# Performance work log

Hardware: AMD Instinct MI355X
Metric: run time of the kernel (lower is better)

Reference implementation:

```python
import jax, jax.numpy as jnp
import numpy as np

H_DIM = 128
C_DIM = 128


def _linear_params(key, in_dim, out_dim):
    kw, kb = jax.random.split(key)
    bound = 1.0 / np.sqrt(in_dim)
    W = jax.random.uniform(kw, (in_dim, out_dim), minval=-bound, maxval=bound, dtype=jnp.float32)
    b = jax.random.uniform(kb, (out_dim,), minval=-bound, maxval=bound, dtype=jnp.float32)
    return W, b


def setup_inputs() -> dict:
    key = jax.random.key(0)
    kx, kh, kc, k1, k2, k3, k4, k5 = jax.random.split(key, 8)
    B = 262144
    x = jax.random.normal(kx, (B, H_DIM), dtype=jnp.float32)
    h = jax.random.normal(kh, (B, H_DIM), dtype=jnp.float32)
    c = jax.random.normal(kc, (B, C_DIM), dtype=jnp.float32)
    Wf, bf = _linear_params(k1, 2 * H_DIM, H_DIM)
    Wi, bi = _linear_params(k2, 2 * H_DIM, H_DIM)
    Wc, bc = _linear_params(k3, 2 * H_DIM, C_DIM)
    Wo, bo = _linear_params(k4, 2 * H_DIM, H_DIM)
    Wch, bch = _linear_params(k5, C_DIM, H_DIM)
    return {"x": x, "h": h, "c": c,
            "Wf": Wf, "bf": bf, "Wi": Wi, "bi": bi,
            "Wc": Wc, "bc": bc, "Wo": Wo, "bo": bo,
            "Wch": Wch, "bch": bch}


def reference(x, h, c, Wf, bf, Wi, bi, Wc, bc, Wo, bo, Wch, bch):
    concat = jnp.concatenate([x, h], axis=-1)  # [B, 2H]
    # Fuse the four gate projections into one GEMM, then split.
    W_gates = jnp.concatenate([Wf, Wi, Wc, Wo], axis=1)  # [2H, 3H+C]
    b_gates = jnp.concatenate([bf, bi, bc, bo], axis=0)
    gates = concat @ W_gates + b_gates
    f_pre, i_pre, ct_pre, o_pre = jnp.split(
        gates, [H_DIM, 2 * H_DIM, 2 * H_DIM + C_DIM], axis=-1)
    f = jax.nn.sigmoid(f_pre)
    i = jax.nn.sigmoid(i_pre)
    c_tilde = jnp.tanh(ct_pre)
    c_new = f * c + i * c_tilde
    o = jax.nn.sigmoid(o_pre)
    h_new = o * jnp.tanh(c_new @ Wch + bch)
    return (h_new, c_new)
```

## Files before the change

### kernel.cpp

```cpp
#include <hip/hip_runtime.h>
#include <hip/hip_bf16.h>


typedef __attribute__((ext_vector_type(8))) short bf16x8;
typedef __attribute__((ext_vector_type(4))) float f32x4;

#define AB0   0
#define AB1   16384
#define LAND0 32768
#define LAND1 65536
#define CEX0  98304
#define CEX1  106496

static __device__ __forceinline__ unsigned short f2bf(float f) {
    unsigned int u = __builtin_bit_cast(unsigned int, f);
    u += 0x7FFFu + ((u >> 16) & 1u);
    return (unsigned short)(u >> 16);
}

static __device__ __forceinline__ unsigned int cvtpk(float lo, float hi) {
    unsigned int r;
    asm("v_cvt_pk_bf16_f32 %0, %1, %2" : "=v"(r) : "v"(lo), "v"(hi));
    return r;
}

static __device__ __forceinline__ bf16x8 cvt8(f32x4 a, f32x4 b) {
    union { bf16x8 v; unsigned int w[4]; } r;
    r.w[0] = cvtpk(a[0], a[1]);
    r.w[1] = cvtpk(a[2], a[3]);
    r.w[2] = cvtpk(b[0], b[1]);
    r.w[3] = cvtpk(b[2], b[3]);
    return r.v;
}

static __device__ __forceinline__ float fsig(float x) {
    float e = __builtin_amdgcn_exp2f(-1.44269504f * x);
    return __builtin_amdgcn_rcpf(1.0f + e);
}
static __device__ __forceinline__ float ftanh(float x) {
    float e = __builtin_amdgcn_exp2f(2.8853900818f * x);
    return 1.0f - 2.0f * __builtin_amdgcn_rcpf(e + 1.0f);
}

static __device__ __forceinline__ void gload16(const void* gsrc, void* ldst) {
    __builtin_amdgcn_global_load_lds(
        (const __attribute__((address_space(1))) unsigned int*)gsrc,
        (__attribute__((address_space(3))) unsigned int*)ldst,
        16, 0, 0);
}

#define MEMFENCE asm volatile("" ::: "memory")

__global__ void prep_weights(const float* __restrict__ Wf, const float* __restrict__ Wi,
                             const float* __restrict__ Wc, const float* __restrict__ Wo,
                             const float* __restrict__ Wch,
                             unsigned short* __restrict__ WgF,
                             unsigned short* __restrict__ WchF)
{
    int u = blockIdx.x * 256 + threadIdx.x;
    if (u < 16384) {
        int lane = u & 63, g = (u >> 6) & 3, wn = (u >> 8) & 7, ks = u >> 11;
        int l15 = lane & 15, lg = lane >> 4;
        int cg = wn * 16 + l15;
        int k0 = ks * 32 + lg * 8;
        const float* W = (g == 0) ? Wf : (g == 1) ? Wi : (g == 2) ? Wc : Wo;
        union { bf16x8 v; unsigned short s[8]; } r;
#pragma unroll
        for (int i = 0; i < 8; ++i) r.s[i] = f2bf(W[(size_t)(k0 + i) * 128 + cg]);
        *(bf16x8*)(WgF + (size_t)u * 8) = r.v;
    } else if (u < 16384 + 2048) {
        int u2 = u - 16384;
        int lane = u2 & 63, wn = (u2 >> 6) & 7, kt = u2 >> 9;
        int l15 = lane & 15, lg = lane >> 4;
        int col = wn * 16 + l15, k0 = kt * 32 + lg * 8;
        union { bf16x8 v; unsigned short s[8]; } r;
#pragma unroll
        for (int i = 0; i < 8; ++i) r.s[i] = f2bf(Wch[(size_t)(k0 + i) * 128 + col]);
        *(bf16x8*)(WchF + (size_t)u2 * 8) = r.v;
    }
}

#define TILE_BODY(T, CUR, CIN, COUT)                                            \
  do {                                                                          \
    const long m0 = base + (long)(T) * 32;                                      \
                                             \
    if ((T) < 31) {                                                             \
      const char* ln = lds + ((CUR) ? LAND0 : LAND1) + rowA * 1024;             \
      f32x4 q0 = *(const f32x4*)(ln + (((kgA * 4 + 0) ^ swzA) << 4));           \
      f32x4 q1 = *(const f32x4*)(ln + (((kgA * 4 + 1) ^ swzA) << 4));           \
      f32x4 q2 = *(const f32x4*)(ln + (((kgA * 4 + 2) ^ swzA) << 4));           \
      f32x4 q3 = *(const f32x4*)(ln + (((kgA * 4 + 3) ^ swzA) << 4));           \
      char* fb = lds + ((CUR) ? AB0 : AB1);                                     \
      *(bf16x8*)(fb + aoff0) = cvt8(q0, q1);                                    \
      *(bf16x8*)(fb + aoff1) = cvt8(q2, q3);                                    \
    }                                                                           \
    MEMFENCE;                                                                   \
                                \
    if ((T) < 31) {                                                             \
      _Pragma("unroll")                                                         \
      for (int am = 0; am < 2; ++am)                                            \
        _Pragma("unroll")                                                       \
        for (int r = 0; r < 4; ++r)                                             \
          COUT[am * 4 + r] = cg[(m0 + 32 + am * 16 + lg * 4 + r) * 128 + colc]; \
    }                                                                           \
    MEMFENCE;                                                                   \
                                          \
    if ((T) < 30) {                                                             \
      char* ad = lds + ((CUR) ? LAND1 : LAND0) + wn * 1024 + lane * 16;         \
      _Pragma("unroll")                                                         \
      for (int j = 0; j < 4; ++j)                                               \
        gload16(dmaA + (m0 + 64 + wn + j * 8) * 128, ad + j * 8192);            \
    }                                                                           \
    MEMFENCE;                                                                   \
                        \
    {                                                                           \
      const char* ab = lds + ((CUR) ? AB1 : AB0);                               \
      _Pragma("unroll")                                                         \
      for (int ks = 0; ks < 8; ++ks) {                                          \
        bf16x8 af0 = *(const bf16x8*)(ab + ks * 1024 + ((lane * 16) ^ (ks << 4)));       \
        bf16x8 af1 = *(const bf16x8*)(ab + (8 + ks) * 1024 + ((lane * 16) ^ (ks << 4))); \
        _Pragma("unroll")                                                       \
        for (int g_ = 0; g_ < 4; ++g_) {                                        \
          acc[0][g_] = __builtin_amdgcn_mfma_f32_16x16x32_bf16(af0, Breg[ks][g_], acc[0][g_], 0, 0, 0); \
          acc[1][g_] = __builtin_amdgcn_mfma_f32_16x16x32_bf16(af1, Breg[ks][g_], acc[1][g_], 0, 0, 0); \
        }                                                                       \
      }                                                                         \
    }                                                                           \
              \
    {                                                                           \
      char* cexb = lds + ((CUR) ? CEX1 : CEX0);                                 \
      _Pragma("unroll")                                                         \
      for (int am = 0; am < 2; ++am)                                            \
        _Pragma("unroll")                                                       \
        for (int r = 0; r < 4; ++r) {                                           \
          float f_  = fsig(acc[am][0][r] + bfb);                                \
          float i_  = fsig(acc[am][1][r] + bib);                                \
          float ct_ = ftanh(acc[am][2][r] + bcb);                               \
          float cv_ = f_ * CIN[am * 4 + r] + i_ * ct_;                          \
          coutp[(m0 + am * 16 + lg * 4 + r) * 128 + colc] = cv_;                \
          *(unsigned short*)(cexb + (am * 4 + (wn >> 1)) * 1024                 \
               + (cslotbase + lg * 4 + r) * 16 + (l15 & 7) * 2) = f2bf(cv_);    \
        }                                                                       \
    }                                                                           \
       \
    asm volatile("s_waitcnt lgkmcnt(0) vmcnt(8)" ::: "memory");                 \
    __builtin_amdgcn_sched_barrier(0);                                          \
    __builtin_amdgcn_s_barrier();                                               \
    __builtin_amdgcn_sched_barrier(0);                                          \
                                  \
    {                                                                           \
      const char* cexr = lds + ((CUR) ? CEX1 : CEX0);                           \
      f32x4 acc2_0 = {0.f,0.f,0.f,0.f}, acc2_1 = {0.f,0.f,0.f,0.f};             \
      _Pragma("unroll")                                                         \
      for (int kt = 0; kt < 4; ++kt) {                                          \
        bf16x8 p0 = *(const bf16x8*)(cexr + kt * 1024 + lane * 16);             \
        bf16x8 p1 = *(const bf16x8*)(cexr + (4 + kt) * 1024 + lane * 16);       \
        acc2_0 = __builtin_amdgcn_mfma_f32_16x16x32_bf16(p0, Wreg[kt], acc2_0, 0, 0, 0); \
        acc2_1 = __builtin_amdgcn_mfma_f32_16x16x32_bf16(p1, Wreg[kt], acc2_1, 0, 0, 0); \
      }                                                                         \
      _Pragma("unroll")                                                         \
      for (int r = 0; r < 4; ++r) {                                             \
        float o0 = fsig(acc[0][3][r] + bob);                                    \
        houtp[(m0 +      lg * 4 + r) * 128 + colc] = o0 * ftanh(acc2_0[r] + bchb); \
        float o1 = fsig(acc[1][3][r] + bob);                                    \
        houtp[(m0 + 16 + lg * 4 + r) * 128 + colc] = o1 * ftanh(acc2_1[r] + bchb); \
      }                                                                         \
    }                                                                           \
    _Pragma("unroll")                                                           \
    for (int am = 0; am < 2; ++am)                                              \
      _Pragma("unroll")                                                         \
      for (int g_ = 0; g_ < 4; ++g_) acc[am][g_] = (f32x4){0.f,0.f,0.f,0.f};    \
  } while (0)

__global__ __launch_bounds__(512, 2) void lstm_fused(
    const float* __restrict__ xg, const float* __restrict__ hg, const float* __restrict__ cg,
    const float* __restrict__ bfv, const float* __restrict__ biv,
    const float* __restrict__ bcv, const float* __restrict__ bov,
    const float* __restrict__ bchv,
    const unsigned short* __restrict__ WgF, const unsigned short* __restrict__ WchF,
    float* __restrict__ out, int nrows)
{
    __shared__ uint4 lds4[7168];
    char* lds = (char*)lds4;

    const int tid  = threadIdx.x;
    const int lane = tid & 63;
    const int wn   = tid >> 6;
    const int l15  = lane & 15;
    const int lg   = lane >> 4;
    const long base = (long)blockIdx.x << 10;

    float* houtp = out;
    float* coutp = out + (size_t)nrows * 128;

    const int colc = wn * 16 + l15;
    const float bfb = bfv[colc], bib = biv[colc], bcb = bcv[colc],
                bob = bov[colc], bchb = bchv[colc];
    const int cslotbase = ((wn & 1) * 2 + (l15 >> 3)) * 16;

    bf16x8 Breg[8][4];
#pragma unroll
    for (int ks = 0; ks < 8; ++ks)
#pragma unroll
        for (int g = 0; g < 4; ++g)
            Breg[ks][g] = *(const bf16x8*)(WgF + (size_t)((ks * 32 + wn * 4 + g) * 512 + lane * 8));
    bf16x8 Wreg[4];
#pragma unroll
    for (int kt = 0; kt < 4; ++kt)
        Wreg[kt] = *(const bf16x8*)(WchF + (size_t)((kt * 8 + wn) * 512 + lane * 8));

    const int gu = lane ^ wn;
    const float* dmaA = ((gu < 32) ? (xg + gu * 4) : (hg + (gu - 32) * 4));

    const int rowA = tid >> 4;
    const int kgA  = tid & 15;
    const int swzA = rowA & 7;
    const int ksA  = kgA >> 1;
    const int lgA  = (kgA & 1) * 2;
    const int amA  = rowA >> 4;
    const int l15A = rowA & 15;
    const int aoff0 = (amA * 8 + ksA) * 1024 + ((((lgA    ) * 16 + l15A) * 16) ^ (ksA << 4));
    const int aoff1 = (amA * 8 + ksA) * 1024 + ((((lgA + 1) * 16 + l15A) * 16) ^ (ksA << 4));
    const float* asrc = (kgA < 8) ? (xg + kgA * 16) : (hg + (kgA - 8) * 16);

    float c0[8], c1[8];
#pragma unroll
    for (int am = 0; am < 2; ++am)
#pragma unroll
        for (int r = 0; r < 4; ++r)
            c0[am * 4 + r] = cg[(base + am * 16 + lg * 4 + r) * 128 + colc];
    MEMFENCE;
    {
        char* ad = lds + LAND1 + wn * 1024 + lane * 16;
#pragma unroll
        for (int j = 0; j < 4; ++j)
            gload16(dmaA + (base + 32 + wn + j * 8) * 128, ad + j * 8192);
    }
    MEMFENCE;
    {
        const float* s = asrc + (base + rowA) * 128;
        f32x4 v0 = ((const f32x4*)s)[0], v1 = ((const f32x4*)s)[1],
              v2 = ((const f32x4*)s)[2], v3 = ((const f32x4*)s)[3];
        *(bf16x8*)(lds + AB0 + aoff0) = cvt8(v0, v1);
        *(bf16x8*)(lds + AB0 + aoff1) = cvt8(v2, v3);
    }
    asm volatile("s_waitcnt lgkmcnt(0) vmcnt(0)" ::: "memory");
    __builtin_amdgcn_sched_barrier(0);
    __builtin_amdgcn_s_barrier();
    __builtin_amdgcn_sched_barrier(0);

    f32x4 acc[2][4];
#pragma unroll
    for (int am = 0; am < 2; ++am)
#pragma unroll
        for (int g = 0; g < 4; ++g) acc[am][g] = {0.f, 0.f, 0.f, 0.f};

#pragma unroll 1
    for (int t = 0; t < 32; t += 2) {
        TILE_BODY(t,     0, c0, c1);
        TILE_BODY(t + 1, 1, c1, c0);
    }
}

extern "C" void kernel_launch(void* const* d_in, const int* in_sizes, int n_in,
                              void* d_out, int out_size, void* d_ws, size_t ws_size,
                              hipStream_t stream)
{
    const float* x   = (const float*)d_in[0];
    const float* h   = (const float*)d_in[1];
    const float* c   = (const float*)d_in[2];
    const float* Wf  = (const float*)d_in[3];
    const float* bf_ = (const float*)d_in[4];
    const float* Wi  = (const float*)d_in[5];
    const float* bi_ = (const float*)d_in[6];
    const float* Wc  = (const float*)d_in[7];
    const float* bc_ = (const float*)d_in[8];
    const float* Wo  = (const float*)d_in[9];
    const float* bo_ = (const float*)d_in[10];
    const float* Wch = (const float*)d_in[11];
    const float* bch = (const float*)d_in[12];

    unsigned short* WgF  = (unsigned short*)d_ws;
    unsigned short* WchF = WgF + 512 * 256;
    float* out = (float*)d_out;

    int nrows = in_sizes[0] / 128;

    prep_weights<<<dim3(72), dim3(256), 0, stream>>>(Wf, Wi, Wc, Wo, Wch, WgF, WchF);
    lstm_fused<<<dim3(nrows / 1024), dim3(512), 0, stream>>>(
        x, h, c, bf_, bi_, bc_, bo_, bch, WgF, WchF, out, nrows);
}
```

Baseline: 143.4 us.

## Split gate GEMM across 16 waves and exchange activated gates through LDS

Doubles the block to 1024 threads (16 waves). Each wave now computes two 16-column slices of a single gate for 32 rows, where before each wave held all four gates for one column slice. Activated gates are written to LDS as bf16 and regathered per column, so the cell update and output GEMM are split over row halves. The aim is to cut per-wave register pressure, since the weight fragments held per wave drop by half and the Wch weights are now loaded from global inside the loop, and to raise latency hiding. The cost is an extra LDS exchange and barrier per tile, and gate values are rounded to bf16 before the cell update.

```diff
diff --git a/kernel.cpp b/kernel.cpp
--- a/kernel.cpp
+++ b/kernel.cpp
@@ -9,8 +9,8 @@
 #define AB1   16384
 #define LAND0 32768
 #define LAND1 65536
-#define CEX0  98304
-#define CEX1  106496
+#define GEX   98304
+#define CEX   131072
 
 static __device__ __forceinline__ unsigned short f2bf(float f) {
     unsigned int u = __builtin_bit_cast(unsigned int, f);
@@ -33,6 +33,13 @@
     return r.v;
 }
 
+static __device__ __forceinline__ float bf2f_lo(unsigned int u) {
+    return __builtin_bit_cast(float, u << 16);
+}
+static __device__ __forceinline__ float bf2f_hi(unsigned int u) {
+    return __builtin_bit_cast(float, u & 0xFFFF0000u);
+}
+
 static __device__ __forceinline__ float fsig(float x) {
     float e = __builtin_amdgcn_exp2f(-1.44269504f * x);
     return __builtin_amdgcn_rcpf(1.0f + e);
@@ -54,25 +61,27 @@
 __global__ void prep_weights(const float* __restrict__ Wf, const float* __restrict__ Wi,
                              const float* __restrict__ Wc, const float* __restrict__ Wo,
                              const float* __restrict__ Wch,
-                             unsigned short* __restrict__ WgF,
+                             unsigned short* __restrict__ WgF2,
                              unsigned short* __restrict__ WchF)
 {
     int u = blockIdx.x * 256 + threadIdx.x;
     if (u < 16384) {
-        int lane = u & 63, g = (u >> 6) & 3, wn = (u >> 8) & 7, ks = u >> 11;
+        int lane = u & 63, rest = u >> 6;
+        int ks = rest & 7, cf = (rest >> 3) & 1, wvp = rest >> 4;
+        int g1 = wvp & 3, cg = wvp >> 2;
         int l15 = lane & 15, lg = lane >> 4;
-        int cg = wn * 16 + l15;
+        int colg = cg * 32 + cf * 16 + l15;
         int k0 = ks * 32 + lg * 8;
-        const float* W = (g == 0) ? Wf : (g == 1) ? Wi : (g == 2) ? Wc : Wo;
+        const float* W = (g1 == 0) ? Wf : (g1 == 1) ? Wi : (g1 == 2) ? Wc : Wo;
         union { bf16x8 v; unsigned short s[8]; } r;
 #pragma unroll
-        for (int i = 0; i < 8; ++i) r.s[i] = f2bf(W[(size_t)(k0 + i) * 128 + cg]);
-        *(bf16x8*)(WgF + (size_t)u * 8) = r.v;
+        for (int i = 0; i < 8; ++i) r.s[i] = f2bf(W[(size_t)(k0 + i) * 128 + colg]);
+        *(bf16x8*)(WgF2 + (size_t)u * 8) = r.v;
     } else if (u < 16384 + 2048) {
         int u2 = u - 16384;
-        int lane = u2 & 63, wn = (u2 >> 6) & 7, kt = u2 >> 9;
+        int lane = u2 & 63, c8 = (u2 >> 6) & 7, kt = u2 >> 9;
         int l15 = lane & 15, lg = lane >> 4;
-        int col = wn * 16 + l15, k0 = kt * 32 + lg * 8;
+        int col = c8 * 16 + l15, k0 = kt * 32 + lg * 8;
         union { bf16x8 v; unsigned short s[8]; } r;
 #pragma unroll
         for (int i = 0; i < 8; ++i) r.s[i] = f2bf(Wch[(size_t)(k0 + i) * 128 + col]);
@@ -80,180 +89,182 @@
     }
 }
 
-#define TILE_BODY(T, CUR, CIN, COUT)                                            \
+#define TILE_BODY(T, P, CIN, COUT)                                              \
   do {                                                                          \
     const long m0 = base + (long)(T) * 32;                                      \
-                                             \
+         \
     if ((T) < 31) {                                                             \
-      const char* ln = lds + ((CUR) ? LAND0 : LAND1) + rowA * 1024;             \
-      f32x4 q0 = *(const f32x4*)(ln + (((kgA * 4 + 0) ^ swzA) << 4));           \
-      f32x4 q1 = *(const f32x4*)(ln + (((kgA * 4 + 1) ^ swzA) << 4));           \
-      f32x4 q2 = *(const f32x4*)(ln + (((kgA * 4 + 2) ^ swzA) << 4));           \
-      f32x4 q3 = *(const f32x4*)(ln + (((kgA * 4 + 3) ^ swzA) << 4));           \
-      char* fb = lds + ((CUR) ? AB0 : AB1);                                     \
-      *(bf16x8*)(fb + aoff0) = cvt8(q0, q1);                                    \
-      *(bf16x8*)(fb + aoff1) = cvt8(q2, q3);                                    \
+      const char* lnb = lds + ((P) ? LAND0 : LAND1) + rowC * 1024;              \
+      f32x4 q0 = *(const f32x4*)(lnb + (((u0C    ) ^ swzC) << 4));              \
+      f32x4 q1 = *(const f32x4*)(lnb + (((u0C + 1) ^ swzC) << 4));              \
+      *(bf16x8*)(lds + ((P) ? AB0 : AB1) + aoffC) = cvt8(q0, q1);               \
     }                                                                           \
     MEMFENCE;                                                                   \
-                                \
+                                         \
     if ((T) < 31) {                                                             \
       _Pragma("unroll")                                                         \
-      for (int am = 0; am < 2; ++am)                                            \
-        _Pragma("unroll")                                                       \
-        for (int r = 0; r < 4; ++r)                                             \
-          COUT[am * 4 + r] = cg[(m0 + 32 + am * 16 + lg * 4 + r) * 128 + colc]; \
+      for (int r = 0; r < 4; ++r)                                               \
+        COUT[r] = cg[(m0 + 32 + rh * 16 + lg * 4 + r) * 128 + colc2];           \
     }                                                                           \
     MEMFENCE;                                                                   \
                                           \
     if ((T) < 30) {                                                             \
-      char* ad = lds + ((CUR) ? LAND1 : LAND0) + wn * 1024 + lane * 16;         \
-      _Pragma("unroll")                                                         \
-      for (int j = 0; j < 4; ++j)                                               \
-        gload16(dmaA + (m0 + 64 + wn + j * 8) * 128, ad + j * 8192);            \
+      _Pragma("unroll")                                                         \
+      for (int j = 0; j < 2; ++j)                                               \
+        gload16(dmaA + (m0 + 64 + j * 16 + wv) * 128,                           \
+                lds + ((P) ? LAND1 : LAND0) + (j * 16 + wv) * 1024 + lane * 16);\
     }                                                                           \
     MEMFENCE;                                                                   \
-                        \
+                      \
+    f32x4 a00 = {0.f,0.f,0.f,0.f}, a01 = {0.f,0.f,0.f,0.f};                     \
+    f32x4 a10 = {0.f,0.f,0.f,0.f}, a11 = {0.f,0.f,0.f,0.f};                     \
     {                                                                           \
-      const char* ab = lds + ((CUR) ? AB1 : AB0);                               \
+      const char* ab = lds + ((P) ? AB1 : AB0);                                 \
       _Pragma("unroll")                                                         \
       for (int ks = 0; ks < 8; ++ks) {                                          \
         bf16x8 af0 = *(const bf16x8*)(ab + ks * 1024 + ((lane * 16) ^ (ks << 4)));       \
         bf16x8 af1 = *(const bf16x8*)(ab + (8 + ks) * 1024 + ((lane * 16) ^ (ks << 4))); \
-        _Pragma("unroll")                                                       \
-        for (int g_ = 0; g_ < 4; ++g_) {                                        \
-          acc[0][g_] = __builtin_amdgcn_mfma_f32_16x16x32_bf16(af0, Breg[ks][g_], acc[0][g_], 0, 0, 0); \
-          acc[1][g_] = __builtin_amdgcn_mfma_f32_16x16x32_bf16(af1, Breg[ks][g_], acc[1][g_], 0, 0, 0); \
-        }                                                                       \
+        a00 = __builtin_amdgcn_mfma_f32_16x16x32_bf16(af0, Breg[ks][0], a00, 0, 0, 0);   \
+        a01 = __builtin_amdgcn_mfma_f32_16x16x32_bf16(af0, Breg[ks][1], a01, 0, 0, 0);   \
+        a10 = __builtin_amdgcn_mfma_f32_16x16x32_bf16(af1, Breg[ks][0], a10, 0, 0, 0);   \
+        a11 = __builtin_amdgcn_mfma_f32_16x16x32_bf16(af1, Breg[ks][1], a11, 0, 0, 0);   \
       }                                                                         \
     }                                                                           \
-              \
-    {                                                                           \
-      char* cexb = lds + ((CUR) ? CEX1 : CEX0);                                 \
-      _Pragma("unroll")                                                         \
-      for (int am = 0; am < 2; ++am)                                            \
-        _Pragma("unroll")                                                       \
-        for (int r = 0; r < 4; ++r) {                                           \
-          float f_  = fsig(acc[am][0][r] + bfb);                                \
-          float i_  = fsig(acc[am][1][r] + bib);                                \
-          float ct_ = ftanh(acc[am][2][r] + bcb);                               \
-          float cv_ = f_ * CIN[am * 4 + r] + i_ * ct_;                          \
-          coutp[(m0 + am * 16 + lg * 4 + r) * 128 + colc] = cv_;                \
-          *(unsigned short*)(cexb + (am * 4 + (wn >> 1)) * 1024                 \
-               + (cslotbase + lg * 4 + r) * 16 + (l15 & 7) * 2) = f2bf(cv_);    \
-        }                                                                       \
-    }                                                                           \
-       \
-    asm volatile("s_waitcnt lgkmcnt(0) vmcnt(8)" ::: "memory");                 \
+                        \
+    _Pragma("unroll")                                                           \
+    for (int r4 = 0; r4 < 4; ++r4) {                                            \
+      int rA = lg * 4 + r4, rB = 16 + lg * 4 + r4;                              \
+      *(unsigned short*)(lds + GEX + rA * 1024 + gxc0) =                        \
+          f2bf(actM * fsig(actK * (a00[r4] + bb0)) + actC);                     \
+      *(unsigned short*)(lds + GEX + rA * 1024 + gxc1) =                        \
+          f2bf(actM * fsig(actK * (a01[r4] + bb1)) + actC);                     \
+      *(unsigned short*)(lds + GEX + rB * 1024 + gxc0) =                        \
+          f2bf(actM * fsig(actK * (a10[r4] + bb0)) + actC);                     \
+      *(unsigned short*)(lds + GEX + rB * 1024 + gxc1) =                        \
+          f2bf(actM * fsig(actK * (a11[r4] + bb1)) + actC);                     \
+    }                                                                           \
+                               \
+    asm volatile("s_waitcnt lgkmcnt(0)" ::: "memory");                          \
     __builtin_amdgcn_sched_barrier(0);                                          \
     __builtin_amdgcn_s_barrier();                                               \
     __builtin_amdgcn_sched_barrier(0);                                          \
-                                  \
+         \
+    float ok0, ok1, ok2, ok3;                                                   \
     {                                                                           \
-      const char* cexr = lds + ((CUR) ? CEX1 : CEX0);                           \
-      f32x4 acc2_0 = {0.f,0.f,0.f,0.f}, acc2_1 = {0.f,0.f,0.f,0.f};             \
+      _Pragma("unroll")                                                         \
+      for (int r4 = 0; r4 < 4; ++r4) {                                          \
+        int row = rh * 16 + lg * 4 + r4;                                        \
+        uint2 gv = *(const uint2*)(lds + GEX + row * 1024 + colc2 * 8);         \
+        float f_ = bf2f_lo(gv.x), i_ = bf2f_hi(gv.x);                           \
+        float ct_ = bf2f_lo(gv.y), o_ = bf2f_hi(gv.y);                          \
+        float cv_ = f_ * CIN[r4] + i_ * ct_;                                    \
+        coutp[(m0 + row) * 128 + colc2] = cv_;                                  \
+        *(unsigned short*)(lds + cexWB + (lg * 4 + r4) * 16) = f2bf(cv_);       \
+        if (r4 == 0) ok0 = o_; else if (r4 == 1) ok1 = o_;                      \
+        else if (r4 == 2) ok2 = o_; else ok3 = o_;                              \
+      }                                                                         \
+    }                                                                           \
+           \
+    asm volatile("s_waitcnt lgkmcnt(0) vmcnt(4)" ::: "memory");                 \
+    __builtin_amdgcn_sched_barrier(0);                                          \
+    __builtin_amdgcn_s_barrier();                                               \
+    __builtin_amdgcn_sched_barrier(0);                                          \
+                        \
+    {                                                                           \
+      f32x4 acc2 = {0.f, 0.f, 0.f, 0.f};                                        \
       _Pragma("unroll")                                                         \
       for (int kt = 0; kt < 4; ++kt) {                                          \
-        bf16x8 p0 = *(const bf16x8*)(cexr + kt * 1024 + lane * 16);             \
-        bf16x8 p1 = *(const bf16x8*)(cexr + (4 + kt) * 1024 + lane * 16);       \
-        acc2_0 = __builtin_amdgcn_mfma_f32_16x16x32_bf16(p0, Wreg[kt], acc2_0, 0, 0, 0); \
-        acc2_1 = __builtin_amdgcn_mfma_f32_16x16x32_bf16(p1, Wreg[kt], acc2_1, 0, 0, 0); \
+        bf16x8 w = *(const bf16x8*)(WchF + (size_t)((kt * 8 + cg2) * 512 + lane * 8)); \
+        bf16x8 p = *(const bf16x8*)(lds + CEX + (rh * 4 + kt) * 1024 + lane * 16);     \
+        acc2 = __builtin_amdgcn_mfma_f32_16x16x32_bf16(p, w, acc2, 0, 0, 0);    \
       }                                                                         \
-      _Pragma("unroll")                                                         \
-      for (int r = 0; r < 4; ++r) {                                             \
-        float o0 = fsig(acc[0][3][r] + bob);                                    \
-        houtp[(m0 +      lg * 4 + r) * 128 + colc] = o0 * ftanh(acc2_0[r] + bchb); \
-        float o1 = fsig(acc[1][3][r] + bob);                                    \
-        houtp[(m0 + 16 + lg * 4 + r) * 128 + colc] = o1 * ftanh(acc2_1[r] + bchb); \
-      }                                                                         \
-    }                                                                           \
-    _Pragma("unroll")                                                           \
-    for (int am = 0; am < 2; ++am)                                              \
-      _Pragma("unroll")                                                         \
-      for (int g_ = 0; g_ < 4; ++g_) acc[am][g_] = (f32x4){0.f,0.f,0.f,0.f};    \
+      houtp[(m0 + rh * 16 + lg * 4 + 0) * 128 + colc2] = ok0 * ftanh(acc2[0] + bchb); \
+      houtp[(m0 + rh * 16 + lg * 4 + 1) * 128 + colc2] = ok1 * ftanh(acc2[1] + bchb); \
+      houtp[(m0 + rh * 16 + lg * 4 + 2) * 128 + colc2] = ok2 * ftanh(acc2[2] + bchb); \
+      houtp[(m0 + rh * 16 + lg * 4 + 3) * 128 + colc2] = ok3 * ftanh(acc2[3] + bchb); \
+    }                                                                           \
   } while (0)
 
-__global__ __launch_bounds__(512, 2) void lstm_fused(
+__global__ __launch_bounds__(1024, 4) void lstm_fused(
     const float* __restrict__ xg, const float* __restrict__ hg, const float* __restrict__ cg,
     const float* __restrict__ bfv, const float* __restrict__ biv,
     const float* __restrict__ bcv, const float* __restrict__ bov,
     const float* __restrict__ bchv,
-    const unsigned short* __restrict__ WgF, const unsigned short* __restrict__ WchF,
+    const unsigned short* __restrict__ WgF2, const unsigned short* __restrict__ WchF,
     float* __restrict__ out, int nrows)
 {
-    __shared__ uint4 lds4[7168];
+    __shared__ uint4 lds4[8704];
     char* lds = (char*)lds4;
 
     const int tid  = threadIdx.x;
     const int lane = tid & 63;
-    const int wn   = tid >> 6;
+    const int wv   = tid >> 6;
     const int l15  = lane & 15;
     const int lg   = lane >> 4;
+    const int g1   = wv & 3;
+    const int cgp  = wv >> 2;
+    const int rh   = wv >> 3;
+    const int cg2  = wv & 7;
     const long base = (long)blockIdx.x << 10;
 
     float* houtp = out;
     float* coutp = out + (size_t)nrows * 128;
 
-    const int colc = wn * 16 + l15;
-    const float bfb = bfv[colc], bib = biv[colc], bcb = bcv[colc],
-                bob = bov[colc], bchb = bchv[colc];
-    const int cslotbase = ((wn & 1) * 2 + (l15 >> 3)) * 16;
-
-    bf16x8 Breg[8][4];
-#pragma unroll
-    for (int ks = 0; ks < 8; ++ks)
-#pragma unroll
-        for (int g = 0; g < 4; ++g)
-            Breg[ks][g] = *(const bf16x8*)(WgF + (size_t)((ks * 32 + wn * 4 + g) * 512 + lane * 8));
-    bf16x8 Wreg[4];
-#pragma unroll
-    for (int kt = 0; kt < 4; ++kt)
-        Wreg[kt] = *(const bf16x8*)(WchF + (size_t)((kt * 8 + wn) * 512 + lane * 8));
-
-    const int gu = lane ^ wn;
+    const int colc2 = cg2 * 16 + l15;
+    const float bchb = bchv[colc2];
+
+    const float* bsrc = (g1 == 0) ? bfv : (g1 == 1) ? biv : (g1 == 2) ? bcv : bov;
+    const float bb0 = bsrc[cgp * 32 + l15];
+    const float bb1 = bsrc[cgp * 32 + 16 + l15];
+    const float actK = (g1 == 2) ? 2.f : 1.f;
+    const float actM = (g1 == 2) ? 2.f : 1.f;
+    const float actC = (g1 == 2) ? -1.f : 0.f;
+
+    const int gxc0 = (cgp * 32 + l15) * 8 + g1 * 2;
+    const int gxc1 = (cgp * 32 + 16 + l15) * 8 + g1 * 2;
+    const int cexWB = CEX + (rh * 4 + (cg2 >> 1)) * 1024
+                    + ((cg2 & 1) * 2 + (l15 >> 3)) * 256 + (l15 & 7) * 2;
+
+    bf16x8 Breg[8][2];
+#pragma unroll
+    for (int ks = 0; ks < 8; ++ks) {
+        Breg[ks][0] = *(const bf16x8*)(WgF2 + (size_t)((wv * 16 + 0 * 8 + ks) * 512 + lane * 8));
+        Breg[ks][1] = *(const bf16x8*)(WgF2 + (size_t)((wv * 16 + 1 * 8 + ks) * 512 + lane * 8));
+    }
+
+    const int gu = lane ^ (wv & 7);
     const float* dmaA = ((gu < 32) ? (xg + gu * 4) : (hg + (gu - 32) * 4));
 
-    const int rowA = tid >> 4;
-    const int kgA  = tid & 15;
-    const int swzA = rowA & 7;
-    const int ksA  = kgA >> 1;
-    const int lgA  = (kgA & 1) * 2;
-    const int amA  = rowA >> 4;
-    const int l15A = rowA & 15;
-    const int aoff0 = (amA * 8 + ksA) * 1024 + ((((lgA    ) * 16 + l15A) * 16) ^ (ksA << 4));
-    const int aoff1 = (amA * 8 + ksA) * 1024 + ((((lgA + 1) * 16 + l15A) * 16) ^ (ksA << 4));
-    const float* asrc = (kgA < 8) ? (xg + kgA * 16) : (hg + (kgA - 8) * 16);
-
-    float c0[8], c1[8];
-#pragma unroll
-    for (int am = 0; am < 2; ++am)
-#pragma unroll
-        for (int r = 0; r < 4; ++r)
-            c0[am * 4 + r] = cg[(base + am * 16 + lg * 4 + r) * 128 + colc];
+    const int laneC = tid & 63;
+    const int ksC   = (tid >> 6) & 7;
+    const int rfC   = tid >> 9;
+    const int rowC  = rfC * 16 + (laneC & 15);
+    const int swzC  = rowC & 7;
+    const int u0C   = ksC * 8 + (laneC >> 4) * 2;
+    const int aoffC = (rfC * 8 + ksC) * 1024 + ((laneC * 16) ^ (ksC << 4));
+    const int k0C   = ksC * 32 + (laneC >> 4) * 8;
+    const float* asrcC = (k0C < 128) ? (xg + k0C) : (hg + (k0C - 128));
+
+    float c0[4], c1[4];
+#pragma unroll
+    for (int r = 0; r < 4; ++r)
+        c0[r] = cg[(base + rh * 16 + lg * 4 + r) * 128 + colc2];
+    MEMFENCE;
+#pragma unroll
+    for (int j = 0; j < 2; ++j)
+        gload16(dmaA + (base + 32 + j * 16 + wv) * 128,
+                lds + LAND1 + (j * 16 + wv) * 1024 + lane * 16);
     MEMFENCE;
     {
-        char* ad = lds + LAND1 + wn * 1024 + lane * 16;
-#pragma unroll
-        for (int j = 0; j < 4; ++j)
-            gload16(dmaA + (base + 32 + wn + j * 8) * 128, ad + j * 8192);
-    }
-    MEMFENCE;
-    {
-        const float* s = asrc + (base + rowA) * 128;
-        f32x4 v0 = ((const f32x4*)s)[0], v1 = ((const f32x4*)s)[1],
-              v2 = ((const f32x4*)s)[2], v3 = ((const f32x4*)s)[3];
-        *(bf16x8*)(lds + AB0 + aoff0) = cvt8(v0, v1);
-        *(bf16x8*)(lds + AB0 + aoff1) = cvt8(v2, v3);
+        const float* s = asrcC + (base + rowC) * 128;
+        f32x4 q0 = ((const f32x4*)s)[0];
+        f32x4 q1 = ((const f32x4*)s)[1];
+        *(bf16x8*)(lds + AB0 + aoffC) = cvt8(q0, q1);
     }
     asm volatile("s_waitcnt lgkmcnt(0) vmcnt(0)" ::: "memory");
     __builtin_amdgcn_sched_barrier(0);
     __builtin_amdgcn_s_barrier();
     __builtin_amdgcn_sched_barrier(0);
-
-    f32x4 acc[2][4];
-#pragma unroll
-    for (int am = 0; am < 2; ++am)
-#pragma unroll
-        for (int g = 0; g < 4; ++g) acc[am][g] = {0.f, 0.f, 0.f, 0.f};
 
 #pragma unroll 1
     for (int t = 0; t < 32; t += 2) {
@@ -280,13 +291,13 @@
     const float* Wch = (const float*)d_in[11];
     const float* bch = (const float*)d_in[12];
 
-    unsigned short* WgF  = (unsigned short*)d_ws;
-    unsigned short* WchF = WgF + 512 * 256;
+    unsigned short* WgF2 = (unsigned short*)d_ws;
+    unsigned short* WchF = WgF2 + 512 * 256;
     float* out = (float*)d_out;
 
     int nrows = in_sizes[0] / 128;
 
-    prep_weights<<<dim3(72), dim3(256), 0, stream>>>(Wf, Wi, Wc, Wo, Wch, WgF, WchF);
-    lstm_fused<<<dim3(nrows / 1024), dim3(512), 0, stream>>>(
-        x, h, c, bf_, bi_, bc_, bo_, bch, WgF, WchF, out, nrows);
-}
+    prep_weights<<<dim3(72), dim3(256), 0, stream>>>(Wf, Wi, Wc, Wo, Wch, WgF2, WchF);
+    lstm_fused<<<dim3(nrows / 1024), dim3(1024), 0, stream>>>(
+        x, h, c, bf_, bi_, bc_, bo_, bch, WgF2, WchF, out, nrows);
+}
```

New measurement: 396.6 us. 177% more time.
